# Kernel optimization log

Hardware: AMD Instinct MI355X
Metric: run time of the kernel (lower is better)

Reference implementation:

```python
import jax, jax.numpy as jnp
import numpy as np
import math

D_MODEL = 1024
NHEADS = 16
HEAD_DIM = D_MODEL // NHEADS
SEQLEN = 2048
BS = 4


def setup_inputs() -> dict:
    key = jax.random.key(0)
    kq, kk, kv, kwq, kwk, kwv, kwo = jax.random.split(key, 7)
    q = jax.random.normal(kq, (SEQLEN, BS, D_MODEL), dtype=jnp.float32)
    k = jax.random.normal(kk, (SEQLEN, BS, D_MODEL), dtype=jnp.float32)
    v = jax.random.normal(kv, (SEQLEN, BS, D_MODEL), dtype=jnp.float32)
    # proper RoPE table: (seq, head_dim//2, 2) with (cos, sin)
    inv_freq = 1.0 / (10000.0 ** (np.arange(0, HEAD_DIM, 2, dtype=np.float32) / HEAD_DIM))
    angles = np.arange(SEQLEN, dtype=np.float32)[:, None] * inv_freq[None, :]
    freqs_cis = jnp.asarray(np.stack([np.cos(angles), np.sin(angles)], axis=-1))
    scale = 1.0 / math.sqrt(D_MODEL)
    wq = jax.random.normal(kwq, (D_MODEL, D_MODEL), dtype=jnp.float32) * scale
    wk = jax.random.normal(kwk, (D_MODEL, D_MODEL), dtype=jnp.float32) * scale
    wv = jax.random.normal(kwv, (D_MODEL, D_MODEL), dtype=jnp.float32) * scale
    wo = jax.random.normal(kwo, (D_MODEL, D_MODEL), dtype=jnp.float32) * scale
    return {"q": q, "k": k, "v": v, "freqs_cis": freqs_cis,
            "wq": wq, "wk": wk, "wv": wv, "wo": wo}


def _apply_rope(x, fc):
    # x: (L, B, H, hd) -> complex rotation on (hd//2, 2) pairs
    L, B, H, hd = x.shape
    x2 = x.reshape(L, B, H, hd // 2, 2)
    fc = fc[:L].reshape(L, 1, 1, hd // 2, 2)  # broadcast over batch, heads
    real = x2[..., 0] * fc[..., 0] - x2[..., 1] * fc[..., 1]
    imag = x2[..., 1] * fc[..., 0] + x2[..., 0] * fc[..., 1]
    return jnp.stack([real, imag], axis=-1).reshape(L, B, H, hd)


def reference(q, k, v, freqs_cis, wq, wk, wv, wo):
    S, B, D = q.shape
    L = k.shape[0]
    H, hd = NHEADS, HEAD_DIM
    # torch Linear: y = x @ W^T, W: (out, in)
    xq = jnp.einsum('sbd,ed->sbe', q, wq).reshape(S, B, H, hd)
    xk = jnp.einsum('lbd,ed->lbe', k, wk).reshape(L, B, H, hd)
    xv = jnp.einsum('lbd,ed->lbe', v, wv).reshape(L, B, H, hd)
    xq = _apply_rope(xq, freqs_cis)
    xk = _apply_rope(xk, freqs_cis)
    # scores: (B, H, S, L)
    scores = jnp.einsum('sbhd,lbhd->bhsl', xq, xk) / math.sqrt(hd)
    probs = jax.nn.softmax(scores.astype(jnp.float32), axis=-1).astype(xq.dtype)
    out = jnp.einsum('bhsl,lbhd->sbhd', probs, xv).reshape(S, B, H * hd)
    return jnp.einsum('sbe,de->sbd', out, wo)
```

## Files before the change

kernel.cpp:

```cpp
#include <hip/hip_runtime.h>
#include <hip/hip_bf16.h>

#define S_LEN   2048
#define BATCH   4
#define DMODEL  1024
#define NHEADS  16
#define HDIM    64
#define MROWS   (S_LEN * BATCH)

#define NE_ 8388608u
#define WE_ 1048576u

typedef unsigned int uint32;
typedef __attribute__((ext_vector_type(8))) short bf16x8;
typedef __attribute__((ext_vector_type(4))) float f32x4;

__device__ __forceinline__ ushort f2bf(float f) {
    uint32 u = __float_as_uint(f);
    uint32 r = (u + 0x7FFFu + ((u >> 16) & 1u)) >> 16;
    return (ushort)r;
}

__device__ __forceinline__ void gl16(const ushort* g, ushort* l) {
    __builtin_amdgcn_global_load_lds(
        (const __attribute__((address_space(1))) unsigned int*)g,
        (__attribute__((address_space(3))) unsigned int*)l,
        16, 0, 0);
}

__global__ __launch_bounds__(256) void cvt_all(const float* __restrict__ q,
                                               const float* __restrict__ k,
                                               const float* __restrict__ v,
                                               const float* __restrict__ wq,
                                               const float* __restrict__ wk,
                                               const float* __restrict__ wv,
                                               const float* __restrict__ wo,
                                               ushort* __restrict__ ws) {
    int i = blockIdx.x * 256 + threadIdx.x;
    const float* src;
    ushort* dst;
    int j;
    if (i < 3 * 2097152) {
        int t = i >> 21;
        j = i & 2097151;
        src = (t == 0) ? q : (t == 1) ? k : v;
        dst = ws + (size_t)t * NE_;
    } else {
        int u2 = i - 3 * 2097152;
        int t = u2 >> 18;
        j = u2 & 262143;
        src = (t == 0) ? wq : (t == 1) ? wk : (t == 2) ? wv : wo;
        dst = ws + 3 * (size_t)NE_ + (size_t)t * WE_;
    }
    float4 f = ((const float4*)src)[j];
    ushort4 u;
    u.x = f2bf(f.x); u.y = f2bf(f.y); u.z = f2bf(f.z); u.w = f2bf(f.w);
    ((ushort4*)dst)[j] = u;
}

__global__ __launch_bounds__(256) void qk_gemm(const ushort* __restrict__ qb,
                                               const ushort* __restrict__ kb,
                                               const ushort* __restrict__ wqb,
                                               const ushort* __restrict__ wkb,
                                               const float* __restrict__ FC,
                                               ushort* __restrict__ Qh,
                                               ushort* __restrict__ Kh) {
    __shared__ __align__(16) ushort A_lds[128 * 32];
    __shared__ __align__(16) ushort B_lds[128 * 32];

    const int tid  = threadIdx.x;
    const int lane = tid & 63;
    const int wvx  = tid >> 6;
    const int wm   = wvx >> 1, wn = wvx & 1;
    const int quad = lane >> 4, l16 = lane & 15;
    const int pid   = blockIdx.x >> 9;
    const int local = blockIdx.x & 511;
    const int m0 = (local >> 3) * 128;
    const int n0 = (local & 7) * 128;

    const ushort* A = pid ? kb : qb;
    const ushort* W = pid ? wkb : wqb;
    ushort* outb    = pid ? Kh : Qh;

    const int srow = tid >> 2;
    const int scol = (tid & 3) * 8;

    f32x4 acc[4][4] = {};

    for (int k0 = 0; k0 < 1024; k0 += 32) {
        __syncthreads();
        gl16(&A[(size_t)(m0 + srow) * 1024 + k0 + scol],      &A_lds[tid * 8]);
        gl16(&A[(size_t)(m0 + 64 + srow) * 1024 + k0 + scol], &A_lds[2048 + tid * 8]);
        gl16(&W[(size_t)(n0 + srow) * 1024 + k0 + scol],      &B_lds[tid * 8]);
        gl16(&W[(size_t)(n0 + 64 + srow) * 1024 + k0 + scol], &B_lds[2048 + tid * 8]);
        __syncthreads();

        const ushort* Ab = &A_lds[(wm * 64 + l16) * 32 + quad * 8];
        const ushort* Bb = &B_lds[(wn * 64 + l16) * 32 + quad * 8];
        bf16x8 af[4], bfr[4];
#pragma unroll
        for (int i = 0; i < 4; ++i) af[i]  = *(const bf16x8*)(Ab + i * 512);
#pragma unroll
        for (int i = 0; i < 4; ++i) bfr[i] = *(const bf16x8*)(Bb + i * 512);
#pragma unroll
        for (int im = 0; im < 4; ++im)
#pragma unroll
            for (int in = 0; in < 4; ++in)
                acc[im][in] = __builtin_amdgcn_mfma_f32_16x16x32_bf16(
                    af[im], bfr[in], acc[im][in], 0, 0, 0);
    }

#pragma unroll
    for (int im = 0; im < 4; ++im) {
        int mbase = m0 + wm * 64 + im * 16 + quad * 4;
        int s = mbase >> 2;
#pragma unroll
        for (int in = 0; in < 4; ++in) {
            int e = n0 + wn * 64 + in * 16 + l16;
            int h = e >> 6, dd = e & 63;
            float2 cs = *(const float2*)&FC[s * 64 + (dd & ~1)];
            float sgn = (dd & 1) ? 1.0f : -1.0f;
#pragma unroll
            for (int rr = 0; rr < 4; ++rr) {
                float vv = acc[im][in][rr];
                float pp = __shfl_xor(vv, 1, 64);
                float ov = vv * cs.x + sgn * pp * cs.y;
                outb[((size_t)(rr * NHEADS + h) * S_LEN + s) * HDIM + dd] = f2bf(ov);
            }
        }
    }
}

__global__ __launch_bounds__(256) void v_gemm(const ushort* __restrict__ vb,
                                              const ushort* __restrict__ wvb,
                                              ushort* __restrict__ Vt) {
    __shared__ __align__(16) ushort A_lds[128 * 32];
    __shared__ __align__(16) ushort B_lds[128 * 32];

    const int tid  = threadIdx.x;
    const int lane = tid & 63;
    const int wvx  = tid >> 6;
    const int wm   = wvx >> 1, wn = wvx & 1;
    const int quad = lane >> 4, l16 = lane & 15;
    const int m0 = (blockIdx.x >> 3) * 128;
    const int n0 = (blockIdx.x & 7) * 128;

    const int srow = tid >> 2;
    const int scol = (tid & 3) * 8;

    f32x4 acc[4][4] = {};

    for (int k0 = 0; k0 < 1024; k0 += 32) {
        __syncthreads();
        gl16(&vb[(size_t)(m0 + srow) * 1024 + k0 + scol],      &A_lds[tid * 8]);
        gl16(&vb[(size_t)(m0 + 64 + srow) * 1024 + k0 + scol], &A_lds[2048 + tid * 8]);
        gl16(&wvb[(size_t)(n0 + srow) * 1024 + k0 + scol],      &B_lds[tid * 8]);
        gl16(&wvb[(size_t)(n0 + 64 + srow) * 1024 + k0 + scol], &B_lds[2048 + tid * 8]);
        __syncthreads();

        const ushort* Ab = &A_lds[(wm * 64 + l16) * 32 + quad * 8];
        const ushort* Bb = &B_lds[(wn * 64 + l16) * 32 + quad * 8];
        bf16x8 af[4], bfr[4];
#pragma unroll
        for (int i = 0; i < 4; ++i) af[i]  = *(const bf16x8*)(Ab + i * 512);
#pragma unroll
        for (int i = 0; i < 4; ++i) bfr[i] = *(const bf16x8*)(Bb + i * 512);
#pragma unroll
        for (int im = 0; im < 4; ++im)
#pragma unroll
            for (int in = 0; in < 4; ++in)
                acc[im][in] = __builtin_amdgcn_mfma_f32_16x16x32_bf16(
                    af[im], bfr[in], acc[im][in], 0, 0, 0);
    }

#pragma unroll
    for (int im = 0; im < 4; ++im) {
        int mbase = m0 + wm * 64 + im * 16 + quad * 4;
        int s = mbase >> 2;
#pragma unroll
        for (int in = 0; in < 4; ++in) {
            int e = n0 + wn * 64 + in * 16 + l16;
            int h = e >> 6, dd = e & 63;
#pragma unroll
            for (int rr = 0; rr < 4; ++rr) {
                Vt[((size_t)(rr * NHEADS + h) * HDIM + dd) * S_LEN + s] =
                    f2bf(acc[im][in][rr]);
            }
        }
    }
}

__global__ __launch_bounds__(256) void out_gemm(const ushort* __restrict__ A,
                                                const ushort* __restrict__ W,
                                                float* __restrict__ outf) {
    __shared__ __align__(16) ushort A_lds[128 * 32];
    __shared__ __align__(16) ushort B_lds[128 * 32];

    const int tid  = threadIdx.x;
    const int lane = tid & 63;
    const int wvx  = tid >> 6;
    const int wm   = wvx >> 1, wn = wvx & 1;
    const int quad = lane >> 4, l16 = lane & 15;
    const int m0 = (blockIdx.x >> 3) * 128;
    const int n0 = (blockIdx.x & 7) * 128;

    const int srow = tid >> 2;
    const int scol = (tid & 3) * 8;

    f32x4 acc[4][4] = {};

    for (int k0 = 0; k0 < 1024; k0 += 32) {
        __syncthreads();
        gl16(&A[(size_t)(m0 + srow) * 1024 + k0 + scol],      &A_lds[tid * 8]);
        gl16(&A[(size_t)(m0 + 64 + srow) * 1024 + k0 + scol], &A_lds[2048 + tid * 8]);
        gl16(&W[(size_t)(n0 + srow) * 1024 + k0 + scol],      &B_lds[tid * 8]);
        gl16(&W[(size_t)(n0 + 64 + srow) * 1024 + k0 + scol], &B_lds[2048 + tid * 8]);
        __syncthreads();

        const ushort* Ab = &A_lds[(wm * 64 + l16) * 32 + quad * 8];
        const ushort* Bb = &B_lds[(wn * 64 + l16) * 32 + quad * 8];
        bf16x8 af[4], bfr[4];
#pragma unroll
        for (int i = 0; i < 4; ++i) af[i]  = *(const bf16x8*)(Ab + i * 512);
#pragma unroll
        for (int i = 0; i < 4; ++i) bfr[i] = *(const bf16x8*)(Bb + i * 512);
#pragma unroll
        for (int im = 0; im < 4; ++im)
#pragma unroll
            for (int in = 0; in < 4; ++in)
                acc[im][in] = __builtin_amdgcn_mfma_f32_16x16x32_bf16(
                    af[im], bfr[in], acc[im][in], 0, 0, 0);
    }

#pragma unroll
    for (int im = 0; im < 4; ++im) {
        int mbase = m0 + wm * 64 + im * 16 + quad * 4;
#pragma unroll
        for (int in = 0; in < 4; ++in) {
            int e = n0 + wn * 64 + in * 16 + l16;
#pragma unroll
            for (int rr = 0; rr < 4; ++rr)
                outf[(size_t)(mbase + rr) * 1024 + e] = acc[im][in][rr];
        }
    }
}

__global__ __launch_bounds__(256) void attn_mfma(const ushort* __restrict__ Qb,
                                                 const ushort* __restrict__ Kb,
                                                 const ushort* __restrict__ Vt,
                                                 ushort* __restrict__ Ob) {
    __shared__ __align__(16) ushort K_lds[64 * 64];
    __shared__ __align__(16) ushort V_lds[64 * 64];
    __shared__ __align__(16) ushort P_lds[4][32 * 72];

    const int tid  = threadIdx.x;
    const int lane = tid & 63;
    const int wv   = tid >> 6;
    const int quad = lane >> 4;
    const int l16  = lane & 15;
    const int head = blockIdx.x >> 4;
    const int qt   = blockIdx.x & 15;
    const int q0   = qt * 128 + wv * 32;
    const size_t hb = (size_t)head * (S_LEN * HDIM);

    bf16x8 qf[2][2];
#pragma unroll
    for (int im = 0; im < 2; ++im)
#pragma unroll
        for (int kk = 0; kk < 2; ++kk)
            qf[im][kk] = *(const bf16x8*)
                &Qb[hb + (size_t)(q0 + im * 16 + l16) * HDIM + kk * 32 + quad * 8];

    f32x4 o[2][4] = {};
    f32x4 lsum[2] = {};

    const int srow = tid >> 3;
    const int scol = (((tid & 7) ^ (srow & 7)) * 8);
    const int sx   = (l16 & 7) * 8;

    for (int kc = 0; kc < S_LEN; kc += 64) {
        __syncthreads();
        gl16(&Kb[hb + (size_t)(kc + srow) * HDIM + scol],      &K_lds[tid * 8]);
        gl16(&Kb[hb + (size_t)(kc + 32 + srow) * HDIM + scol], &K_lds[2048 + tid * 8]);
        gl16(&Vt[hb + (size_t)srow * S_LEN + kc + scol],        &V_lds[tid * 8]);
        gl16(&Vt[hb + (size_t)(32 + srow) * S_LEN + kc + scol], &V_lds[2048 + tid * 8]);
        __syncthreads();

        f32x4 sc[2][4] = {};
#pragma unroll
        for (int nt = 0; nt < 4; ++nt) {
            bf16x8 kf0 = *(const bf16x8*)&K_lds[(nt * 16 + l16) * 64 + ((quad * 8) ^ sx)];
            bf16x8 kf1 = *(const bf16x8*)&K_lds[(nt * 16 + l16) * 64 + ((32 + quad * 8) ^ sx)];
#pragma unroll
            for (int im = 0; im < 2; ++im) {
                sc[im][nt] = __builtin_amdgcn_mfma_f32_16x16x32_bf16(
                    qf[im][0], kf0, sc[im][nt], 0, 0, 0);
                sc[im][nt] = __builtin_amdgcn_mfma_f32_16x16x32_bf16(
                    qf[im][1], kf1, sc[im][nt], 0, 0, 0);
            }
        }

#pragma unroll
        for (int im = 0; im < 2; ++im) {
#pragma unroll
            for (int nt = 0; nt < 4; ++nt) {
                f32x4 p;
#pragma unroll
                for (int r = 0; r < 4; ++r) p[r] = __expf(sc[im][nt][r] * 0.125f);
                lsum[im] += p;
#pragma unroll
                for (int r = 0; r < 4; ++r) {
                    uint32 u = __float_as_uint(p[r]);
                    P_lds[wv][(im * 16 + quad * 4 + r) * 72 + nt * 16 + l16] =
                        (ushort)((u + 0x8000u) >> 16);
                }
            }
        }
        __builtin_amdgcn_wave_barrier();

        bf16x8 pf[2][2];
#pragma unroll
        for (int im = 0; im < 2; ++im)
#pragma unroll
            for (int kk = 0; kk < 2; ++kk)
                pf[im][kk] = *(const bf16x8*)
                    &P_lds[wv][(im * 16 + l16) * 72 + kk * 32 + quad * 8];
#pragma unroll
        for (int dt = 0; dt < 4; ++dt) {
            bf16x8 vf0 = *(const bf16x8*)&V_lds[(dt * 16 + l16) * 64 + ((quad * 8) ^ sx)];
            bf16x8 vf1 = *(const bf16x8*)&V_lds[(dt * 16 + l16) * 64 + ((32 + quad * 8) ^ sx)];
#pragma unroll
            for (int im = 0; im < 2; ++im) {
                o[im][dt] = __builtin_amdgcn_mfma_f32_16x16x32_bf16(
                    pf[im][0], vf0, o[im][dt], 0, 0, 0);
                o[im][dt] = __builtin_amdgcn_mfma_f32_16x16x32_bf16(
                    pf[im][1], vf1, o[im][dt], 0, 0, 0);
            }
        }
    }

#pragma unroll
    for (int im = 0; im < 2; ++im)
#pragma unroll
        for (int off = 1; off < 16; off <<= 1)
#pragma unroll
            for (int r = 0; r < 4; ++r)
                lsum[im][r] += __shfl_xor(lsum[im][r], off, 64);

    const int b = head >> 4;
    const int h = head & 15;
#pragma unroll
    for (int im = 0; im < 2; ++im) {
        f32x4 inv;
#pragma unroll
        for (int r = 0; r < 4; ++r) inv[r] = 1.0f / lsum[im][r];
#pragma unroll
        for (int dt = 0; dt < 4; ++dt) {
#pragma unroll
            for (int r = 0; r < 4; ++r) {
                int s = q0 + im * 16 + quad * 4 + r;
                Ob[(size_t)(s * BATCH + b) * 1024 + h * HDIM + dt * 16 + l16] =
                    f2bf(o[im][dt][r] * inv[r]);
            }
        }
    }
}

extern "C" void kernel_launch(void* const* d_in, const int* in_sizes, int n_in,
                              void* d_out, int out_size, void* d_ws, size_t ws_size,
                              hipStream_t stream) {
    const float* q   = (const float*)d_in[0];
    const float* k   = (const float*)d_in[1];
    const float* v   = (const float*)d_in[2];
    const float* fc  = (const float*)d_in[3];
    const float* wq  = (const float*)d_in[4];
    const float* wk  = (const float*)d_in[5];
    const float* wvp = (const float*)d_in[6];
    const float* wo  = (const float*)d_in[7];

    ushort* ws = (ushort*)d_ws;
    ushort* qb  = ws;
    ushort* kb  = ws + NE_;
    ushort* vb  = ws + 2 * (size_t)NE_;
    ushort* wqb = ws + 3 * (size_t)NE_;
    ushort* wkb = wqb + WE_;
    ushort* wvb = wqb + 2 * (size_t)WE_;
    ushort* wob = wqb + 3 * (size_t)WE_;

    ushort* Qh = (ushort*)d_out;
    ushort* Kh = Qh + NE_;
    ushort* Vt = ws;
    ushort* R3 = ws + NE_;

    cvt_all<<<28672, 256, 0, stream>>>(q, k, v, wq, wk, wvp, wo, ws);

    qk_gemm<<<1024, 256, 0, stream>>>(qb, kb, wqb, wkb, fc, Qh, Kh);

    v_gemm<<<512, 256, 0, stream>>>(vb, wvb, Vt);

    attn_mfma<<<1024, 256, 0, stream>>>(Qh, Kh, Vt, R3);

    out_gemm<<<512, 256, 0, stream>>>(R3, wob, (float*)d_out);
}
```

Measured before the change: 398.4 us.

## Keep softmax probabilities in registers via transposed MFMA and permuted V layout

Computes S^T = K·Q^T so each lane holds probabilities in the layout needed as the B operand of the PV MFMA. This removes the per-wave P staging through LDS, and V is written by the projection kernel in a permuted sequence order to match. The softmax scale and log2(e) are folded into the Q projection, so raw v_exp_f32 and packed bf16 conversion replace __expf and manual rounding. The output is staged through LDS for 16-byte coalesced stores. Costs include reliance on the exact MFMA lane layout and the permutation's correctness, plus reduced LDS use.

```diff
diff --git a/kernel.cpp b/kernel.cpp
--- a/kernel.cpp
+++ b/kernel.cpp
@@ -19,6 +19,18 @@
     uint32 u = __float_as_uint(f);
     uint32 r = (u + 0x7FFFu + ((u >> 16) & 1u)) >> 16;
     return (ushort)r;
+}
+
+__device__ __forceinline__ uint32 pk_bf16(float a, float b) {
+    uint32 r;
+    asm("v_cvt_pk_bf16_f32 %0, %1, %2" : "=v"(r) : "v"(a), "v"(b));
+    return r;
+}
+
+__device__ __forceinline__ float exp2_asm(float x) {
+    float r;
+    asm("v_exp_f32 %0, %1" : "=v"(r) : "v"(x));
+    return r;
 }
 
 __device__ __forceinline__ void gl16(const ushort* g, ushort* l) {
@@ -81,6 +93,7 @@
     const ushort* A = pid ? kb : qb;
     const ushort* W = pid ? wkb : wqb;
     ushort* outb    = pid ? Kh : Qh;
+    const float osc = pid ? 1.0f : 0.18033688011111793f;
 
     const int srow = tid >> 2;
     const int scol = (tid & 3) * 8;
@@ -124,7 +137,7 @@
             for (int rr = 0; rr < 4; ++rr) {
                 float vv = acc[im][in][rr];
                 float pp = __shfl_xor(vv, 1, 64);
-                float ov = vv * cs.x + sgn * pp * cs.y;
+                float ov = (vv * cs.x + sgn * pp * cs.y) * osc;
                 outb[((size_t)(rr * NHEADS + h) * S_LEN + s) * HDIM + dd] = f2bf(ov);
             }
         }
@@ -177,13 +190,17 @@
     for (int im = 0; im < 4; ++im) {
         int mbase = m0 + wm * 64 + im * 16 + quad * 4;
         int s = mbase >> 2;
+        int nt2 = (s >> 4) & 3;
+        int qd  = (s >> 2) & 3;
+        int r2  = s & 3;
+        int pos = (s & ~63) | ((nt2 >> 1) << 5) | (qd << 3) | ((nt2 & 1) << 2) | r2;
 #pragma unroll
         for (int in = 0; in < 4; ++in) {
             int e = n0 + wn * 64 + in * 16 + l16;
             int h = e >> 6, dd = e & 63;
 #pragma unroll
             for (int rr = 0; rr < 4; ++rr) {
-                Vt[((size_t)(rr * NHEADS + h) * HDIM + dd) * S_LEN + s] =
+                Vt[((size_t)(rr * NHEADS + h) * HDIM + dd) * S_LEN + pos] =
                     f2bf(acc[im][in][rr]);
             }
         }
@@ -249,9 +266,7 @@
                                                  const ushort* __restrict__ Kb,
                                                  const ushort* __restrict__ Vt,
                                                  ushort* __restrict__ Ob) {
-    __shared__ __align__(16) ushort K_lds[64 * 64];
-    __shared__ __align__(16) ushort V_lds[64 * 64];
-    __shared__ __align__(16) ushort P_lds[4][32 * 72];
+    __shared__ __align__(16) ushort KV[8192];
 
     const int tid  = threadIdx.x;
     const int lane = tid & 63;
@@ -272,7 +287,7 @@
                 &Qb[hb + (size_t)(q0 + im * 16 + l16) * HDIM + kk * 32 + quad * 8];
 
     f32x4 o[2][4] = {};
-    f32x4 lsum[2] = {};
+    float lsum[2] = {0.f, 0.f};
 
     const int srow = tid >> 3;
     const int scol = (((tid & 7) ^ (srow & 7)) * 8);
@@ -280,89 +295,85 @@
 
     for (int kc = 0; kc < S_LEN; kc += 64) {
         __syncthreads();
-        gl16(&Kb[hb + (size_t)(kc + srow) * HDIM + scol],      &K_lds[tid * 8]);
-        gl16(&Kb[hb + (size_t)(kc + 32 + srow) * HDIM + scol], &K_lds[2048 + tid * 8]);
-        gl16(&Vt[hb + (size_t)srow * S_LEN + kc + scol],        &V_lds[tid * 8]);
-        gl16(&Vt[hb + (size_t)(32 + srow) * S_LEN + kc + scol], &V_lds[2048 + tid * 8]);
-        __syncthreads();
-
-        f32x4 sc[2][4] = {};
+        gl16(&Kb[hb + (size_t)(kc + srow) * HDIM + scol],      &KV[tid * 8]);
+        gl16(&Kb[hb + (size_t)(kc + 32 + srow) * HDIM + scol], &KV[2048 + tid * 8]);
+        gl16(&Vt[hb + (size_t)srow * S_LEN + kc + scol],        &KV[4096 + tid * 8]);
+        gl16(&Vt[hb + (size_t)(32 + srow) * S_LEN + kc + scol], &KV[4096 + 2048 + tid * 8]);
+        __syncthreads();
+
+        f32x4 st[2][4] = {};
 #pragma unroll
         for (int nt = 0; nt < 4; ++nt) {
-            bf16x8 kf0 = *(const bf16x8*)&K_lds[(nt * 16 + l16) * 64 + ((quad * 8) ^ sx)];
-            bf16x8 kf1 = *(const bf16x8*)&K_lds[(nt * 16 + l16) * 64 + ((32 + quad * 8) ^ sx)];
+            bf16x8 kf0 = *(const bf16x8*)&KV[(nt * 16 + l16) * 64 + ((quad * 8) ^ sx)];
+            bf16x8 kf1 = *(const bf16x8*)&KV[(nt * 16 + l16) * 64 + ((32 + quad * 8) ^ sx)];
 #pragma unroll
             for (int im = 0; im < 2; ++im) {
-                sc[im][nt] = __builtin_amdgcn_mfma_f32_16x16x32_bf16(
-                    qf[im][0], kf0, sc[im][nt], 0, 0, 0);
-                sc[im][nt] = __builtin_amdgcn_mfma_f32_16x16x32_bf16(
-                    qf[im][1], kf1, sc[im][nt], 0, 0, 0);
+                st[im][nt] = __builtin_amdgcn_mfma_f32_16x16x32_bf16(
+                    kf0, qf[im][0], st[im][nt], 0, 0, 0);
+                st[im][nt] = __builtin_amdgcn_mfma_f32_16x16x32_bf16(
+                    kf1, qf[im][1], st[im][nt], 0, 0, 0);
             }
         }
 
+        union { uint32 d[16]; bf16x8 v[4]; } P;
 #pragma unroll
         for (int im = 0; im < 2; ++im) {
+            float ls = 0.f;
 #pragma unroll
             for (int nt = 0; nt < 4; ++nt) {
-                f32x4 p;
-#pragma unroll
-                for (int r = 0; r < 4; ++r) p[r] = __expf(sc[im][nt][r] * 0.125f);
-                lsum[im] += p;
-#pragma unroll
-                for (int r = 0; r < 4; ++r) {
-                    uint32 u = __float_as_uint(p[r]);
-                    P_lds[wv][(im * 16 + quad * 4 + r) * 72 + nt * 16 + l16] =
-                        (ushort)((u + 0x8000u) >> 16);
-                }
+                float p0 = exp2_asm(st[im][nt][0]);
+                float p1 = exp2_asm(st[im][nt][1]);
+                float p2 = exp2_asm(st[im][nt][2]);
+                float p3 = exp2_asm(st[im][nt][3]);
+                ls += (p0 + p1) + (p2 + p3);
+                P.d[im * 8 + nt * 2]     = pk_bf16(p0, p1);
+                P.d[im * 8 + nt * 2 + 1] = pk_bf16(p2, p3);
             }
-        }
-        __builtin_amdgcn_wave_barrier();
-
-        bf16x8 pf[2][2];
-#pragma unroll
-        for (int im = 0; im < 2; ++im)
-#pragma unroll
-            for (int kk = 0; kk < 2; ++kk)
-                pf[im][kk] = *(const bf16x8*)
-                    &P_lds[wv][(im * 16 + l16) * 72 + kk * 32 + quad * 8];
+            lsum[im] += ls;
+        }
+
 #pragma unroll
         for (int dt = 0; dt < 4; ++dt) {
-            bf16x8 vf0 = *(const bf16x8*)&V_lds[(dt * 16 + l16) * 64 + ((quad * 8) ^ sx)];
-            bf16x8 vf1 = *(const bf16x8*)&V_lds[(dt * 16 + l16) * 64 + ((32 + quad * 8) ^ sx)];
+            bf16x8 vf0 = *(const bf16x8*)&KV[4096 + (dt * 16 + l16) * 64 + ((quad * 8) ^ sx)];
+            bf16x8 vf1 = *(const bf16x8*)&KV[4096 + (dt * 16 + l16) * 64 + ((32 + quad * 8) ^ sx)];
 #pragma unroll
             for (int im = 0; im < 2; ++im) {
                 o[im][dt] = __builtin_amdgcn_mfma_f32_16x16x32_bf16(
-                    pf[im][0], vf0, o[im][dt], 0, 0, 0);
+                    vf0, P.v[im * 2], o[im][dt], 0, 0, 0);
                 o[im][dt] = __builtin_amdgcn_mfma_f32_16x16x32_bf16(
-                    pf[im][1], vf1, o[im][dt], 0, 0, 0);
+                    vf1, P.v[im * 2 + 1], o[im][dt], 0, 0, 0);
             }
         }
     }
 
 #pragma unroll
-    for (int im = 0; im < 2; ++im)
-#pragma unroll
-        for (int off = 1; off < 16; off <<= 1)
-#pragma unroll
-            for (int r = 0; r < 4; ++r)
-                lsum[im][r] += __shfl_xor(lsum[im][r], off, 64);
-
-    const int b = head >> 4;
-    const int h = head & 15;
-#pragma unroll
     for (int im = 0; im < 2; ++im) {
-        f32x4 inv;
-#pragma unroll
-        for (int r = 0; r < 4; ++r) inv[r] = 1.0f / lsum[im][r];
+        lsum[im] += __shfl_xor(lsum[im], 16, 64);
+        lsum[im] += __shfl_xor(lsum[im], 32, 64);
+    }
+
+    __syncthreads();
+    ushort* Est = &KV[wv * 2048];
+#pragma unroll
+    for (int im = 0; im < 2; ++im) {
+        float inv = 1.0f / lsum[im];
 #pragma unroll
         for (int dt = 0; dt < 4; ++dt) {
-#pragma unroll
-            for (int r = 0; r < 4; ++r) {
-                int s = q0 + im * 16 + quad * 4 + r;
-                Ob[(size_t)(s * BATCH + b) * 1024 + h * HDIM + dt * 16 + l16] =
-                    f2bf(o[im][dt][r] * inv[r]);
-            }
-        }
+            uint2 w;
+            w.x = pk_bf16(o[im][dt][0] * inv, o[im][dt][1] * inv);
+            w.y = pk_bf16(o[im][dt][2] * inv, o[im][dt][3] * inv);
+            *(uint2*)&Est[(im * 16 + l16) * 64 + dt * 16 + quad * 4] = w;
+        }
+    }
+    __syncthreads();
+
+    const int row  = lane >> 1, half = lane & 1;
+    const int b = head >> 4, h = head & 15;
+    const size_t ob = (size_t)((q0 + row) * BATCH + b) * 1024 + h * 64 + half * 32;
+#pragma unroll
+    for (int e = 0; e < 4; ++e) {
+        bf16x8 t = *(const bf16x8*)&Est[row * 64 + half * 32 + e * 8];
+        *(bf16x8*)&Ob[ob + e * 8] = t;
     }
 }
 
```

Result: faster. 378.0 us (-5.1%).
